# Optimization experiments

Hardware: AMD Instinct MI355X
Metric: run time of the kernel (lower is better)

## Reference

```python
import jax, jax.numpy as jnp
import numpy as np
from jax import lax

DIM = 64        # Branch(dim)
OUT = 2048      # TimesBlock out_channels == TTT model_dim
NH = 8          # num_heads
HD = OUT // NH  # 256 head dim
INNER = 4 * HD  # ttt_mlp hidden
MB = 10         # mini_batch_size
BASE_LR = 0.1   # ttt_base_lr
NK = 6          # TimesBlock num_kernels (k = 1,3,5,7,9,11)
LN_EPS = 1e-6


def _gelu(x):
    return jax.nn.gelu(x, approximate=False)


def _gelu_bwd(x):
    return 0.5 * (1.0 + lax.erf(x / jnp.sqrt(2.0))) + x * jnp.exp(-0.5 * x * x) / jnp.sqrt(2.0 * jnp.pi)


def _ttt_head(qs, ks, vs, W1h, b1h, W2h, b2h, gw, gb):
    # qs/ks/vs: [NC, MB, HD]; sequential scan over mini-batch chunks (TTT inner GD)
    eta = BASE_LR / MB

    def step(carry, chunk):
        W1c, b1c, W2c, b2c = carry
        xq, xk, xv = chunk
        Z1 = xk @ W1c + b1c              # [MB, INNER]
        A1 = _gelu(Z1)
        Z2 = A1 @ W2c + b2c              # [MB, HD]
        # grad of 0.5*||LN(Z2) - (xv - xk)||^2 wrt Z2 (fused LN l2 backward)
        tgt = xv - xk
        mu = Z2.mean(-1, keepdims=True)
        std = jnp.sqrt(Z2.var(-1, keepdims=True) + LN_EPS)
        xhat = (2 * 0 + Z2 - mu) / std
        gout = (gw * xhat + gb) - tgt
        gxh = gout * gw
        gZ2 = (gxh - gxh.mean(-1, keepdims=True) - xhat * (gxh * xhat).mean(-1, keepdims=True)) / std
        gZ1 = (gZ2 @ W2c.T) * _gelu_bwd(Z1)
        # inner-model SGD step
        W1n = W1c - eta * (xk.T @ gZ1)
        b1n = b1c - eta * gZ1.sum(0)
        W2n = W2c - eta * (A1.T @ gZ2)
        b2n = b2c - eta * gZ2.sum(0)
        # apply updated inner model to queries, post-LN + residual
        Z1q = xq @ W1n + b1n
        Z2q = _gelu(Z1q) @ W2n + b2n
        muq = Z2q.mean(-1, keepdims=True)
        stdq = jnp.sqrt(Z2q.var(-1, keepdims=True) + LN_EPS)
        out = xq + gw * ((Z2q - muq) / stdq) + gb
        return (W1n, b1n, W2n, b2n), out

    _, outs = lax.scan(step, (W1h, b1h, W2h, b2h), (qs, ks, vs))
    return outs.reshape(-1, HD)  # [T, HD]


def _forward(x, seg, conv_ws, conv_bs, wq, wk, wv, wo, W1, b1, W2, b2, ln_w, ln_b):
    B, T, C = x.shape
    xg = jnp.transpose(x, (0, 2, 1)).reshape(B, C, T // seg, seg)
    dn = ('NCHW', 'OIHW', 'NCHW')
    acc = 0.0
    for w, bc in zip(conv_ws, conv_bs):
        acc = acc + lax.conv_general_dilated(xg, w, (1, 1), 'SAME', dimension_numbers=dn) + bc[None, :, None, None]
    xb = acc / float(len(conv_ws))            # TimesBlock: mean over kernel ensemble
    xb = jax.nn.silu(xb)
    xb = jnp.transpose(xb.reshape(B, OUT, T), (0, 2, 1))  # [B, T, OUT]

    def heads(h):  # [B,T,OUT] -> [B,NH,NC,MB,HD]
        return jnp.transpose(h.reshape(B, T, NH, HD), (0, 2, 1, 3)).reshape(B, NH, T // MB, MB, HD)

    q = heads(xb @ wq.T)
    k = heads(xb @ wk.T)
    v = heads(xb @ wv.T)
    f = jax.vmap(jax.vmap(_ttt_head, in_axes=(0, 0, 0, 0, 0, 0, 0, 0, 0)),
                 in_axes=(0, 0, 0, None, None, None, None, None, None))
    o = f(q, k, v, W1, b1, W2, b2, ln_w, ln_b)  # [B, NH, T, HD]
    o = jnp.transpose(o, (0, 2, 1, 3)).reshape(B, T, OUT)
    return o @ wo.T


def setup_inputs() -> dict:
    key = jax.random.key(0)
    ks = jax.random.split(key, 24)
    B, T = 2, 400
    inp = {"x": jax.random.normal(ks[0], (B, T, DIM), jnp.float32), "seg": 20}
    for i in range(NK):
        kk = 2 * i + 1
        fan_out = OUT * kk * kk
        inp[f"conv_w{i}"] = jax.random.normal(ks[1 + i], (OUT, DIM, kk, kk), jnp.float32) * np.sqrt(2.0 / fan_out)
        inp[f"conv_b{i}"] = jnp.zeros((OUT,), jnp.float32)
    for j, nm in enumerate(["wq", "wk", "wv", "wo"]):
        inp[nm] = jax.random.normal(ks[8 + j], (OUT, OUT), jnp.float32) * 0.02
    inp["W1"] = jax.random.normal(ks[12], (NH, HD, INNER), jnp.float32) * 0.02
    inp["b1"] = jnp.zeros((NH, INNER), jnp.float32)
    inp["W2"] = jax.random.normal(ks[13], (NH, INNER, HD), jnp.float32) * 0.02
    inp["b2"] = jnp.zeros((NH, HD), jnp.float32)
    inp["ln_w"] = jnp.ones((NH, HD), jnp.float32)
    inp["ln_b"] = jnp.zeros((NH, HD), jnp.float32)
    return inp


def reference(x, seg, conv_w0, conv_b0, conv_w1, conv_b1, conv_w2, conv_b2,
              conv_w3, conv_b3, conv_w4, conv_b4, conv_w5, conv_b5,
              wq, wk, wv, wo, W1, b1, W2, b2, ln_w, ln_b):
    conv_ws = [conv_w0, conv_w1, conv_w2, conv_w3, conv_w4, conv_w5]
    conv_bs = [conv_b0, conv_b1, conv_b2, conv_b3, conv_b4, conv_b5]
    return _forward(x, seg, conv_ws, conv_bs, wq, wk, wv, wo, W1, b1, W2, b2, ln_w, ln_b)
```

## Files before the change

### kernel.cpp

```cpp
#include <hip/hip_runtime.h>


typedef __bf16 bf16x8 __attribute__((ext_vector_type(8)));
typedef float  f32x4  __attribute__((ext_vector_type(4)));

__device__ __forceinline__ unsigned short f2bf(float f){
  unsigned int u = __builtin_bit_cast(unsigned int, f);
  u += 0x7fffu + ((u >> 16) & 1u);
  return (unsigned short)(u >> 16);
}
__device__ __forceinline__ float bf2f(unsigned short b){
  unsigned int u = ((unsigned int)b) << 16;
  return __builtin_bit_cast(float, u);
}
__device__ __forceinline__ float gelu_f(float x){
  return 0.5f * x * (1.0f + erff(x * 0.70710678118654752f));
}
__device__ __forceinline__ float gelu_bwd_f(float x){
  return 0.5f * (1.0f + erff(x * 0.70710678118654752f))
       + x * __expf(-0.5f * x * x) * 0.3989422804014327f;
}

__device__ __forceinline__ float2 aload2(const float* p){
  unsigned long long v = __hip_atomic_load((const unsigned long long*)p,
                                           __ATOMIC_RELAXED, __HIP_MEMORY_SCOPE_AGENT);
  union { unsigned long long u; float2 f; } cv; cv.u = v; return cv.f;
}
__device__ __forceinline__ void aadd(float* p, float v){
  __hip_atomic_fetch_add(p, v, __ATOMIC_RELAXED, __HIP_MEMORY_SCOPE_AGENT);
}


__global__ __launch_bounds__(256) void k_weff(
    const float* __restrict__ w0, const float* __restrict__ w1,
    const float* __restrict__ w2, const float* __restrict__ w3,
    const float* __restrict__ w4, const float* __restrict__ w5,
    unsigned short* __restrict__ weff)
{
  extern __shared__ float sw[];
  const int off[6] = {0, 64, 640, 2240, 5376, 10560};
  const float* ws6[6] = {w0, w1, w2, w3, w4, w5};
  int o = blockIdx.x, tid = threadIdx.x;
#pragma unroll
  for (int i = 0; i < 6; i++){
    int kk = 2 * i + 1, sz = 64 * kk * kk;
    const float* src = ws6[i] + (size_t)o * sz;
    for (int idx = tid; idx < sz; idx += 256) sw[off[i] + idx] = src[idx];
  }
  __syncthreads();
  for (int t = tid; t < 7744; t += 256){
    int c = t / 121, dd = t % 121, di = dd / 11, dj = dd % 11;
    float s = 0.f;
#pragma unroll
    for (int i = 0; i < 6; i++){
      int kk = 2 * i + 1;
      int a = di - 5 + i, b = dj - 5 + i;
      if (a >= 0 && a < kk && b >= 0 && b < kk)
        s += sw[off[i] + (c * kk + a) * kk + b];
    }
    weff[(size_t)o * 7744 + t] = f2bf(s);
  }
}

__global__ __launch_bounds__(256) void k_im2col(
    const float* __restrict__ x, unsigned short* __restrict__ P)
{
  int idx = blockIdx.x * 256 + threadIdx.x;
  if (idx >= 800 * 7744) return;
  int n = idx / 7744, k = idx % 7744;
  int c = k / 121, dd = k % 121, di = dd / 11, dj = dd % 11;
  int b = n / 400, pos = n % 400, i = pos / 20, j = pos % 20;
  int ii = i + di - 5, jj = j + dj - 5;
  float v = 0.f;
  if (ii >= 0 && ii < 20 && jj >= 0 && jj < 20)
    v = x[((size_t)b * 400 + ii * 20 + jj) * 64 + c];
  P[idx] = f2bf(v);
}

__global__ __launch_bounds__(256) void k_wqkv(
    const float* __restrict__ wq, const float* __restrict__ wk,
    const float* __restrict__ wv, unsigned short* __restrict__ dst)
{
  int idx = blockIdx.x * 256 + threadIdx.x;
  if (idx >= 6144 * 2048) return;
  int m = idx >> 11, kk = idx & 2047;
  const float* src = (m < 2048) ? wq : ((m < 4096) ? wk : wv);
  dst[idx] = f2bf(src[(size_t)(m & 2047) * 2048 + kk]);
}

__global__ __launch_bounds__(256) void k_f2bf_copy(
    const float* __restrict__ src, unsigned short* __restrict__ dst, int n)
{
  int idx = blockIdx.x * 256 + threadIdx.x;
  if (idx < n) dst[idx] = f2bf(src[idx]);
}

__global__ __launch_bounds__(256) void k_bsum(
    const float* __restrict__ b0, const float* __restrict__ b1,
    const float* __restrict__ b2, const float* __restrict__ b3,
    const float* __restrict__ b4, const float* __restrict__ b5,
    float* __restrict__ bsum)
{
  int idx = blockIdx.x * 256 + threadIdx.x;
  if (idx < 2048)
    bsum[idx] = b0[idx] + b1[idx] + b2[idx] + b3[idx] + b4[idx] + b5[idx];
}

__global__ __launch_bounds__(256) void k_comb_silu(
    const float* __restrict__ p0, const float* __restrict__ p1,
    const float* __restrict__ bsum, unsigned short* __restrict__ xb)
{
  int i4 = (blockIdx.x * 256 + threadIdx.x) * 4;
  float4 a = *(const float4*)&p0[i4];
  float4 b = *(const float4*)&p1[i4];
  int mm = i4 & 2047;
  float4 bs = *(const float4*)&bsum[mm];
  float v[4] = {a.x + b.x + bs.x, a.y + b.y + bs.y, a.z + b.z + bs.z, a.w + b.w + bs.w};
  ushort4 o;
#pragma unroll
  for (int i = 0; i < 4; i++){
    float t = v[i] * (1.0f / 6.0f);
    float sv = t / (1.0f + __expf(-t));
    ((unsigned short*)&o)[i] = f2bf(sv);
  }
  *(ushort4*)&xb[i4] = o;
}

__global__ __launch_bounds__(256) void k_comb_add4(
    const float* __restrict__ p, float* __restrict__ out)
{
  int i4 = (blockIdx.x * 256 + threadIdx.x) * 4;
  float4 a = *(const float4*)&p[i4];
  float4 b = *(const float4*)&p[1638400 + i4];
  float4 c = *(const float4*)&p[3276800 + i4];
  float4 d = *(const float4*)&p[4915200 + i4];
  float4 o = {a.x + b.x + c.x + d.x, a.y + b.y + c.y + d.y,
              a.z + b.z + c.z + d.z, a.w + b.w + c.w + d.w};
  *(float4*)&out[i4] = o;
}

template<int MODE>
__global__ __launch_bounds__(256, 1) void k_gemm(
    const unsigned short* __restrict__ A, const unsigned short* __restrict__ B,
    int M, int N, int lda, int ldb, int kLen,
    unsigned short* __restrict__ qb, unsigned short* __restrict__ kb,
    unsigned short* __restrict__ vb, float* __restrict__ outf)
{
  __shared__ unsigned short As[128 * 32];
  __shared__ unsigned short Bs[128 * 32];
  int tid = threadIdx.x, w = tid >> 6, l = tid & 63, qd = l >> 4, lm = l & 15;
  int m0 = blockIdx.x * 128, n0 = blockIdx.y * 128;
  int kBase = blockIdx.z * kLen;

  f32x4 acc[4][4];
#pragma unroll
  for (int i = 0; i < 4; i++)
#pragma unroll
    for (int j = 0; j < 4; j++){ acc[i][j][0]=0.f; acc[i][j][1]=0.f; acc[i][j][2]=0.f; acc[i][j][3]=0.f; }

  int nk = kLen >> 5;
  for (int kt = 0; kt < nk; kt++){
    int k0 = kBase + (kt << 5);
#pragma unroll
    for (int i = 0; i < 2; i++){
      int cidx = tid + i * 256;
      int row = cidx >> 2, kc = (cidx & 3) << 3;
      *(uint4*)&As[row * 32 + kc] = *(const uint4*)&A[(size_t)(m0 + row) * lda + k0 + kc];
      int br = n0 + row; if (br >= N) br = N - 1;
      *(uint4*)&Bs[row * 32 + kc] = *(const uint4*)&B[(size_t)br * ldb + k0 + kc];
    }
    __syncthreads();
    bf16x8 af[4], bfv[4];
#pragma unroll
    for (int i = 0; i < 4; i++)
      af[i] = *(const bf16x8*)&As[((w >> 1) * 64 + i * 16 + lm) * 32 + qd * 8];
#pragma unroll
    for (int j = 0; j < 4; j++)
      bfv[j] = *(const bf16x8*)&Bs[((w & 1) * 64 + j * 16 + lm) * 32 + qd * 8];
#pragma unroll
    for (int i = 0; i < 4; i++)
#pragma unroll
      for (int j = 0; j < 4; j++)
        acc[i][j] = __builtin_amdgcn_mfma_f32_16x16x32_bf16(af[i], bfv[j], acc[i][j], 0, 0, 0);
    __syncthreads();
  }

#pragma unroll
  for (int i = 0; i < 4; i++){
    int mBase = m0 + (w >> 1) * 64 + i * 16 + qd * 4;
#pragma unroll
    for (int j = 0; j < 4; j++){
      int n = n0 + (w & 1) * 64 + j * 16 + lm;
      if (n < N){
#pragma unroll
        for (int rr = 0; rr < 4; rr++){
          float val = acc[i][j][rr];
          int mm = mBase + rr;
          if (MODE == 1){
            int proj = mm >> 11, o = mm & 2047, hh = o >> 8, d = o & 255;
            int bh = (n / 400) * 8 + hh, tt = n % 400;
            unsigned short* dst = (proj == 0) ? qb : ((proj == 1) ? kb : vb);
            dst[((size_t)bh * 400 + tt) * 256 + d] = f2bf(val);
          } else {
            outf[(size_t)blockIdx.z * M * N + (size_t)n * M + mm] = val;
          }
        }
      }
    }
  }
}

#define O_W1BT 0
#define O_W2K  16896
#define O_W2N  33792
#define O_XKQ  52224
#define O_TGT  54864
#define O_A1   57424
#define O_A1T  58144
#define O_GZ2  60192
#define O_GZ1  62832
#define O_XQ2  64880
#define O_GZ2T 67520
#define O_XKT  73664
#define O_A1Q  79808
#define O_F32  80528
#define O_GW   81168
#define O_GB   81424
#define US_TOTAL 81680
#define TTT_LDS_BYTES (81680 * 2)

#define ETA 0.01f
#define BAR_STRIDE 32

__global__ __launch_bounds__(256, 1) void k_ttt(
    const unsigned short* __restrict__ qg, const unsigned short* __restrict__ kg,
    const unsigned short* __restrict__ vg,
    const float* __restrict__ W1g, const float* __restrict__ b1g,
    const float* __restrict__ W2g, const float* __restrict__ b2g,
    const float* __restrict__ gwg, const float* __restrict__ gbg,
    float* __restrict__ z2acc, unsigned short* __restrict__ zqp,
    unsigned int* __restrict__ bar)
{
  extern __shared__ unsigned short lds[];
  float* ldsf = (float*)&lds[O_F32];

  int tid = threadIdx.x, w = tid >> 6, l = tid & 63, qd = l >> 4, lm = l & 15;
  int bid = blockIdx.x;
  int jj = bid >> 3, xx = bid & 7;
  int h  = xx + 8 * (jj >> 4);
  int sl = jj & 15;
  int hh = h & 7;

  for (int i = tid; i < US_TOTAL; i += 256) lds[i] = 0;
  __syncthreads();

  float w1r[4][4][4];
#pragma unroll
  for (int a = 0; a < 4; a++)
#pragma unroll
    for (int nt = 0; nt < 4; nt++)
#pragma unroll
      for (int rr = 0; rr < 4; rr++)
        w1r[a][nt][rr] = W1g[((size_t)hh * 256 + (4 * w + a) * 16 + qd * 4 + rr) * 1024
                             + sl * 64 + nt * 16 + lm];
  float w2r[16][4];
#pragma unroll
  for (int nt = 0; nt < 16; nt++)
#pragma unroll
    for (int rr = 0; rr < 4; rr++)
      w2r[nt][rr] = W2g[((size_t)hh * 1024 + sl * 64 + w * 16 + qd * 4 + rr) * 256
                        + nt * 16 + lm];
  if (tid < 64)  ldsf[tid] = b1g[hh * 1024 + sl * 64 + tid];
  if (tid < 256){
    ldsf[64 + tid] = b2g[hh * 256 + tid];
    lds[O_GW + tid] = f2bf(gwg[hh * 256 + tid]);
    lds[O_GB + tid] = f2bf(gbg[hh * 256 + tid]);
  }

#define WRITE_W1BF() do { \
  _Pragma("unroll") for (int a = 0; a < 4; a++){ \
    int m0i = (4 * w + a) * 16 + qd * 4; \
    _Pragma("unroll") for (int nt = 0; nt < 4; nt++){ \
      int n = nt * 16 + lm; \
      unsigned int p0 = f2bf(w1r[a][nt][0]) | ((unsigned int)f2bf(w1r[a][nt][1]) << 16); \
      unsigned int p1 = f2bf(w1r[a][nt][2]) | ((unsigned int)f2bf(w1r[a][nt][3]) << 16); \
      *(unsigned int*)&lds[O_W1BT + n * 264 + m0i]     = p0; \
      *(unsigned int*)&lds[O_W1BT + n * 264 + m0i + 2] = p1; \
    } } } while(0)

#define WRITE_W2BF() do { \
  int mB = w * 16 + qd * 4; \
  _Pragma("unroll") for (int nt = 0; nt < 16; nt++){ \
    int n = nt * 16 + lm; \
    _Pragma("unroll") for (int rr = 0; rr < 4; rr++) \
      lds[O_W2K + (mB + rr) * 264 + n] = f2bf(w2r[nt][rr]); \
    unsigned int p0 = f2bf(w2r[nt][0]) | ((unsigned int)f2bf(w2r[nt][1]) << 16); \
    unsigned int p1 = f2bf(w2r[nt][2]) | ((unsigned int)f2bf(w2r[nt][3]) << 16); \
    *(unsigned int*)&lds[O_W2N + n * 72 + mB]     = p0; \
    *(unsigned int*)&lds[O_W2N + n * 72 + mB + 2] = p1; \
  } } while(0)

  const size_t hb2 = (size_t)h * 400 * 256;

#define LOAD_XK_TGT(NCH) do { \
  const unsigned int* kp = (const unsigned int*)(kg + hb2 + (size_t)(NCH) * 2560); \
  const unsigned int* vp = (const unsigned int*)(vg + hb2 + (size_t)(NCH) * 2560); \
  _Pragma("unroll") for (int i5 = 0; i5 < 5; i5++){ \
    int f2i = i5 * 256 + tid; \
    unsigned int ku = kp[f2i], vu = vp[f2i]; \
    int row = f2i >> 7, col = (f2i & 127) * 2; \
    *(unsigned int*)&lds[O_XKQ + row * 264 + col] = ku; \
    lds[O_XKT + col * 24 + row]       = (unsigned short)(ku & 0xffffu); \
    lds[O_XKT + (col + 1) * 24 + row] = (unsigned short)(ku >> 16); \
    float kv0 = bf2f((unsigned short)(ku & 0xffffu)), kv1 = bf2f((unsigned short)(ku >> 16)); \
    float vv0 = bf2f((unsigned short)(vu & 0xffffu)), vv1 = bf2f((unsigned short)(vu >> 16)); \
    unsigned int tu = (unsigned int)f2bf(vv0 - kv0) | ((unsigned int)f2bf(vv1 - kv1) << 16); \
    *(unsigned int*)&lds[O_TGT + row * 256 + col] = tu; \
  } } while(0)

#define LOAD_XQ(NCH) do { \
  const unsigned int* qp = (const unsigned int*)(qg + hb2 + (size_t)(NCH) * 2560); \
  _Pragma("unroll") for (int i5 = 0; i5 < 5; i5++){ \
    int f2i = i5 * 256 + tid; \
    unsigned int qu = qp[f2i]; \
    int row = f2i >> 7, col = (f2i & 127) * 2; \
    *(unsigned int*)&lds[O_XQ2 + row * 264 + col] = qu; \
  } } while(0)

  WRITE_W1BF();
  WRITE_W2BF();
  LOAD_XK_TGT(0);
  LOAD_XQ(0);
  __syncthreads();

  for (int nch = 0; nch < 40; nch++){
    const size_t chunkBase = (size_t)(h * 40 + nch) * 10 * 256;

    f32x4 z1a; z1a[0]=0.f; z1a[1]=0.f; z1a[2]=0.f; z1a[3]=0.f;
#pragma unroll
    for (int ks = 0; ks < 8; ks++){
      bf16x8 av = *(const bf16x8*)&lds[O_XKQ + lm * 264 + ks * 32 + qd * 8];
      bf16x8 bv = *(const bf16x8*)&lds[O_W1BT + (w * 16 + lm) * 264 + ks * 32 + qd * 8];
      z1a = __builtin_amdgcn_mfma_f32_16x16x32_bf16(av, bv, z1a, 0, 0, 0);
    }
    float z1v[4];
    {
      float b1n = ldsf[w * 16 + lm];
#pragma unroll
      for (int rr = 0; rr < 4; rr++){
        z1v[rr] = z1a[rr] + b1n;
        int mr = qd * 4 + rr;
        if (mr < 10){
          float a1 = gelu_f(z1v[rr]);
          unsigned short ab = f2bf(a1);
          lds[O_A1 + mr * 72 + w * 16 + lm] = ab;
          lds[O_A1T + (w * 16 + lm) * 32 + mr] = ab;
        }
      }
    }
    __syncthreads();

#pragma unroll
    for (int nt4 = 0; nt4 < 4; nt4++){
      int nt = 4 * w + nt4;
      f32x4 p; p[0]=0.f; p[1]=0.f; p[2]=0.f; p[3]=0.f;
#pragma unroll
      for (int ks = 0; ks < 2; ks++){
        bf16x8 av = *(const bf16x8*)&lds[O_A1 + lm * 72 + ks * 32 + qd * 8];
        bf16x8 bv = *(const bf16x8*)&lds[O_W2N + (nt * 16 + lm) * 72 + ks * 32 + qd * 8];
        p = __builtin_amdgcn_mfma_f32_16x16x32_bf16(av, bv, p, 0, 0, 0);
      }
#pragma unroll
      for (int rr = 0; rr < 4; rr++){
        int mr = qd * 4 + rr;
        if (mr < 10)
          aadd(&z2acc[chunkBase + (size_t)mr * 256 + nt * 16 + lm], p[rr]);
      }
    }
    __syncthreads();

    if (tid == 0)
      __hip_atomic_fetch_add(bar + h * BAR_STRIDE, 1u, __ATOMIC_RELAXED, __HIP_MEMORY_SCOPE_AGENT);

    if (nch > 0){
      f32x4 zq; zq[0]=0.f; zq[1]=0.f; zq[2]=0.f; zq[3]=0.f;
#pragma unroll
      for (int ks = 0; ks < 8; ks++){
        bf16x8 av = *(const bf16x8*)&lds[O_XQ2 + lm * 264 + ks * 32 + qd * 8];
        bf16x8 bv = *(const bf16x8*)&lds[O_W1BT + (w * 16 + lm) * 264 + ks * 32 + qd * 8];
        zq = __builtin_amdgcn_mfma_f32_16x16x32_bf16(av, bv, zq, 0, 0, 0);
      }
      float b1n = ldsf[w * 16 + lm];
#pragma unroll
      for (int rr = 0; rr < 4; rr++){
        int mr = qd * 4 + rr;
        if (mr < 10)
          lds[O_A1Q + mr * 72 + w * 16 + lm] = f2bf(gelu_f(zq[rr] + b1n));
      }
    }
    __syncthreads();

    if (nch > 0){
      LOAD_XQ(nch);
      unsigned short* zq_out = zqp + ((size_t)(h * 16 + sl) * 40 + (nch - 1)) * 2560;
#pragma unroll
      for (int nt4 = 0; nt4 < 4; nt4++){
        int nt = 4 * w + nt4;
        f32x4 p; p[0]=0.f; p[1]=0.f; p[2]=0.f; p[3]=0.f;
#pragma unroll
        for (int ks = 0; ks < 2; ks++){
          bf16x8 av = *(const bf16x8*)&lds[O_A1Q + lm * 72 + ks * 32 + qd * 8];
          bf16x8 bv = *(const bf16x8*)&lds[O_W2N + (nt * 16 + lm) * 72 + ks * 32 + qd * 8];
          p = __builtin_amdgcn_mfma_f32_16x16x32_bf16(av, bv, p, 0, 0, 0);
        }
        float bb = (sl == 0) ? ldsf[64 + nt * 16 + lm] : 0.f;
#pragma unroll
        for (int rr = 0; rr < 4; rr++){
          int mr = qd * 4 + rr;
          if (mr < 10)
            zq_out[mr * 256 + nt * 16 + lm] = f2bf(p[rr] + bb);
        }
      }
    }

    if (tid == 0){
      unsigned int target = 16u * (unsigned int)(nch + 1);
      unsigned int spins = 0;
      while (__hip_atomic_load(bar + h * BAR_STRIDE, __ATOMIC_RELAXED, __HIP_MEMORY_SCOPE_AGENT) < target
             && spins < 8000000u){ spins++; __builtin_amdgcn_s_sleep(1); }
    }
    __syncthreads();

    for (int r2 = w; r2 < 10; r2 += 4){
      int c0 = l * 4;
      const float* bp = &z2acc[chunkBase + (size_t)r2 * 256 + c0];
      float2 u01 = aload2(bp);
      float2 u23 = aload2(bp + 2);
      float zz[4] = {u01.x, u01.y, u23.x, u23.y};
      float s1 = 0.f, s2 = 0.f;
#pragma unroll
      for (int i = 0; i < 4; i++){ zz[i] += ldsf[64 + c0 + i]; s1 += zz[i]; s2 += zz[i] * zz[i]; }
#pragma unroll
      for (int off = 32; off >= 1; off >>= 1){ s1 += __shfl_xor(s1, off, 64); s2 += __shfl_xor(s2, off, 64); }
      float mu = s1 * (1.f / 256.f);
      float var = s2 * (1.f / 256.f) - mu * mu;
      float rstd = rsqrtf(var + 1e-6f);
      float xh[4], gx[4];
      float t1 = 0.f, t2 = 0.f;
#pragma unroll
      for (int i = 0; i < 4; i++){
        xh[i] = (zz[i] - mu) * rstd;
        float gwv = bf2f(lds[O_GW + c0 + i]), gbv = bf2f(lds[O_GB + c0 + i]);
        float tg = bf2f(lds[O_TGT + r2 * 256 + c0 + i]);
        float go = gwv * xh[i] + gbv - tg;
        gx[i] = go * gwv;
        t1 += gx[i]; t2 += gx[i] * xh[i];
      }
#pragma unroll
      for (int off = 32; off >= 1; off >>= 1){ t1 += __shfl_xor(t1, off, 64); t2 += __shfl_xor(t2, off, 64); }
      float m1 = t1 * (1.f / 256.f), m2 = t2 * (1.f / 256.f);
      float g0 = (gx[0] - m1 - xh[0] * m2) * rstd;
      float g1 = (gx[1] - m1 - xh[1] * m2) * rstd;
      float g2 = (gx[2] - m1 - xh[2] * m2) * rstd;
      float g3 = (gx[3] - m1 - xh[3] * m2) * rstd;
      unsigned int p0 = f2bf(g0) | ((unsigned int)f2bf(g1) << 16);
      unsigned int p1 = f2bf(g2) | ((unsigned int)f2bf(g3) << 16);
      *(unsigned int*)&lds[O_GZ2 + r2 * 264 + c0]     = p0;
      *(unsigned int*)&lds[O_GZ2 + r2 * 264 + c0 + 2] = p1;
    }
    __syncthreads();

    {
      float sum = 0.f;
#pragma unroll
      for (int r2 = 0; r2 < 10; r2++){
        unsigned short g = lds[O_GZ2 + r2 * 264 + tid];
        lds[O_GZ2T + tid * 24 + r2] = g;
        sum += bf2f(g);
      }
      ldsf[64 + tid] -= ETA * sum;
    }
    {
      f32x4 g1a; g1a[0]=0.f; g1a[1]=0.f; g1a[2]=0.f; g1a[3]=0.f;
#pragma unroll
      for (int ks = 0; ks < 8; ks++){
        bf16x8 av = *(const bf16x8*)&lds[O_GZ2 + lm * 264 + ks * 32 + qd * 8];
        bf16x8 bv = *(const bf16x8*)&lds[O_W2K + (w * 16 + lm) * 264 + ks * 32 + qd * 8];
        g1a = __builtin_amdgcn_mfma_f32_16x16x32_bf16(av, bv, g1a, 0, 0, 0);
      }
#pragma unroll
      for (int rr = 0; rr < 4; rr++){
        int mr = qd * 4 + rr;
        if (mr < 10){
          float gz1 = g1a[rr] * gelu_bwd_f(z1v[rr]);
          lds[O_GZ1 + (w * 16 + lm) * 32 + mr] = f2bf(gz1);
        }
      }
    }
    __syncthreads();

    if (tid < 64){
      float sum = 0.f;
#pragma unroll
      for (int kx = 0; kx < 10; kx++) sum += bf2f(lds[O_GZ1 + tid * 32 + kx]);
      ldsf[tid] -= ETA * sum;
    }
#pragma unroll
    for (int a = 0; a < 4; a++){
      int mt = 4 * w + a;
      bf16x8 av = *(const bf16x8*)&lds[O_XKT + (mt * 16 + lm) * 24 + (qd & 1) * 8];
#pragma unroll
      for (int nt = 0; nt < 4; nt++){
        bf16x8 bv = *(const bf16x8*)&lds[O_GZ1 + (nt * 16 + lm) * 32 + qd * 8];
        f32x4 d; d[0]=0.f; d[1]=0.f; d[2]=0.f; d[3]=0.f;
        d = __builtin_amdgcn_mfma_f32_16x16x32_bf16(av, bv, d, 0, 0, 0);
#pragma unroll
        for (int rr = 0; rr < 4; rr++) w1r[a][nt][rr] -= ETA * d[rr];
      }
    }
    {
      bf16x8 av2 = *(const bf16x8*)&lds[O_A1T + (w * 16 + lm) * 32 + qd * 8];
#pragma unroll
      for (int nt = 0; nt < 16; nt++){
        bf16x8 bv = *(const bf16x8*)&lds[O_GZ2T + (nt * 16 + lm) * 24 + (qd & 1) * 8];
        f32x4 d; d[0]=0.f; d[1]=0.f; d[2]=0.f; d[3]=0.f;
        d = __builtin_amdgcn_mfma_f32_16x16x32_bf16(av2, bv, d, 0, 0, 0);
#pragma unroll
        for (int rr = 0; rr < 4; rr++) w2r[nt][rr] -= ETA * d[rr];
      }
    }
    WRITE_W1BF();
    WRITE_W2BF();
    __syncthreads();

    if (nch + 1 < 40){
      LOAD_XK_TGT(nch + 1);
    }
    __syncthreads();
  }

  {
    f32x4 zq; zq[0]=0.f; zq[1]=0.f; zq[2]=0.f; zq[3]=0.f;
#pragma unroll
    for (int ks = 0; ks < 8; ks++){
      bf16x8 av = *(const bf16x8*)&lds[O_XQ2 + lm * 264 + ks * 32 + qd * 8];
      bf16x8 bv = *(const bf16x8*)&lds[O_W1BT + (w * 16 + lm) * 264 + ks * 32 + qd * 8];
      zq = __builtin_amdgcn_mfma_f32_16x16x32_bf16(av, bv, zq, 0, 0, 0);
    }
    float b1n = ldsf[w * 16 + lm];
#pragma unroll
    for (int rr = 0; rr < 4; rr++){
      int mr = qd * 4 + rr;
      if (mr < 10)
        lds[O_A1Q + mr * 72 + w * 16 + lm] = f2bf(gelu_f(zq[rr] + b1n));
    }
  }
  __syncthreads();
  {
    unsigned short* zq_out = zqp + ((size_t)(h * 16 + sl) * 40 + 39) * 2560;
#pragma unroll
    for (int nt4 = 0; nt4 < 4; nt4++){
      int nt = 4 * w + nt4;
      f32x4 p; p[0]=0.f; p[1]=0.f; p[2]=0.f; p[3]=0.f;
#pragma unroll
      for (int ks = 0; ks < 2; ks++){
        bf16x8 av = *(const bf16x8*)&lds[O_A1Q + lm * 72 + ks * 32 + qd * 8];
        bf16x8 bv = *(const bf16x8*)&lds[O_W2N + (nt * 16 + lm) * 72 + ks * 32 + qd * 8];
        p = __builtin_amdgcn_mfma_f32_16x16x32_bf16(av, bv, p, 0, 0, 0);
      }
      float bb = (sl == 0) ? ldsf[64 + nt * 16 + lm] : 0.f;
#pragma unroll
      for (int rr = 0; rr < 4; rr++){
        int mr = qd * 4 + rr;
        if (mr < 10)
          zq_out[mr * 256 + nt * 16 + lm] = f2bf(p[rr] + bb);
      }
    }
  }
}

__global__ __launch_bounds__(256) void k_lnout(
    const unsigned short* __restrict__ zqp, const unsigned short* __restrict__ qg,
    const float* __restrict__ gwg, const float* __restrict__ gbg,
    unsigned short* __restrict__ obf)
{
  int w = threadIdx.x >> 6, l = threadIdx.x & 63;
  int gr = blockIdx.x * 4 + w;
  int h = gr / 400, t = gr % 400, hh = h & 7, b = h >> 3;
  int nch = t / 10, mr = t % 10;
  int c0 = l * 4;
  float z[4] = {0.f, 0.f, 0.f, 0.f};
#pragma unroll
  for (int sl = 0; sl < 16; sl++){
    const unsigned short* zp = zqp + (((size_t)(h * 16 + sl) * 40 + nch) * 10 + mr) * 256 + c0;
    ushort4 u = *(const ushort4*)zp;
    z[0] += bf2f(u.x); z[1] += bf2f(u.y); z[2] += bf2f(u.z); z[3] += bf2f(u.w);
  }
  float s1 = 0.f, s2 = 0.f;
#pragma unroll
  for (int i = 0; i < 4; i++){ s1 += z[i]; s2 += z[i] * z[i]; }
#pragma unroll
  for (int off = 32; off >= 1; off >>= 1){ s1 += __shfl_xor(s1, off, 64); s2 += __shfl_xor(s2, off, 64); }
  float mu = s1 * (1.f / 256.f);
  float var = s2 * (1.f / 256.f) - mu * mu;
  float rstd = rsqrtf(var + 1e-6f);
  const unsigned short* qp = &qg[((size_t)h * 400 + t) * 256];
  ushort4 qu = *(const ushort4*)&qp[c0];
  float qv[4] = {bf2f(qu.x), bf2f(qu.y), bf2f(qu.z), bf2f(qu.w)};
  unsigned short* op = &obf[((size_t)(b * 400 + t)) * 2048 + hh * 256];
#pragma unroll
  for (int i = 0; i < 4; i++){
    float xh = (z[i] - mu) * rstd;
    float o = qv[i] + gwg[hh * 256 + c0 + i] * xh + gbg[hh * 256 + c0 + i];
    op[c0 + i] = f2bf(o);
  }
}

#define WS_WEFF   0u
#define WS_P      31719424u
#define WS_WQKV   44109824u
#define WS_WOB    52428800u
#define WS_Z2ACC  62722048u
#define WS_XB     69275648u
#define WS_Q      72552448u
#define WS_K      75829248u
#define WS_V      79106048u
#define WS_OBF    82382848u
#define WS_BSUM   85659648u
#define WS_BAR    85667840u

extern "C" void kernel_launch(void* const* d_in, const int* in_sizes, int n_in,
                              void* d_out, int out_size, void* d_ws, size_t ws_size,
                              hipStream_t stream)
{
  (void)in_sizes; (void)n_in; (void)out_size; (void)ws_size;
  const float* x  = (const float*)d_in[0];
  const float* cw[6]; const float* cb[6];
  for (int i = 0; i < 6; i++){ cw[i] = (const float*)d_in[2 + 2 * i]; cb[i] = (const float*)d_in[3 + 2 * i]; }
  const float* wq  = (const float*)d_in[14];
  const float* wk  = (const float*)d_in[15];
  const float* wv  = (const float*)d_in[16];
  const float* wo  = (const float*)d_in[17];
  const float* W1  = (const float*)d_in[18];
  const float* b1  = (const float*)d_in[19];
  const float* W2  = (const float*)d_in[20];
  const float* b2  = (const float*)d_in[21];
  const float* lnw = (const float*)d_in[22];
  const float* lnb = (const float*)d_in[23];
  float* outf = (float*)d_out;

  char* wsb = (char*)d_ws;
  unsigned short* weff = (unsigned short*)(wsb + WS_WEFF);
  unsigned short* P    = (unsigned short*)(wsb + WS_P);
  unsigned short* wqkv = (unsigned short*)(wsb + WS_WQKV);
  unsigned short* wob  = (unsigned short*)(wsb + WS_WOB);
  unsigned short* xb   = (unsigned short*)(wsb + WS_XB);
  unsigned short* qb   = (unsigned short*)(wsb + WS_Q);
  unsigned short* kb   = (unsigned short*)(wsb + WS_K);
  unsigned short* vb   = (unsigned short*)(wsb + WS_V);
  float* z2acc = (float*)(wsb + WS_Z2ACC);
  unsigned short* zqp = (unsigned short*)(wsb + WS_WEFF);
  unsigned short* obf = (unsigned short*)(wsb + WS_OBF);
  float* bsum = (float*)(wsb + WS_BSUM);
  unsigned int* bar = (unsigned int*)(wsb + WS_BAR);
  float* g0part = (float*)(wsb + WS_Q);
  float* g2part = (float*)(wsb + WS_WEFF);

  hipMemsetAsync(bar, 0, 16 * BAR_STRIDE * 4, stream);
  hipFuncSetAttribute(reinterpret_cast<const void*>(k_ttt),
                      hipFuncAttributeMaxDynamicSharedMemorySize, TTT_LDS_BYTES);
  hipFuncSetAttribute(reinterpret_cast<const void*>(k_weff),
                      hipFuncAttributeMaxDynamicSharedMemorySize, 18304 * 4);

  k_weff<<<2048, 256, 18304 * 4, stream>>>(cw[0], cw[1], cw[2], cw[3], cw[4], cw[5], weff);
  k_im2col<<<(800 * 7744 + 255) / 256, 256, 0, stream>>>(x, P);
  k_wqkv<<<(6144 * 2048 + 255) / 256, 256, 0, stream>>>(wq, wk, wv, wqkv);
  k_bsum<<<8, 256, 0, stream>>>(cb[0], cb[1], cb[2], cb[3], cb[4], cb[5], bsum);

  k_gemm<2><<<dim3(16, 7, 2), 256, 0, stream>>>(weff, P, 2048, 800, 7744, 7744, 3872,
                                                nullptr, nullptr, nullptr, g0part);
  k_comb_silu<<<1600, 256, 0, stream>>>(g0part, g0part + 1638400, bsum, xb);

  k_gemm<1><<<dim3(48, 7, 1), 256, 0, stream>>>(wqkv, xb, 6144, 800, 2048, 2048, 2048,
                                                qb, kb, vb, nullptr);

  k_f2bf_copy<<<(2048 * 2048 + 255) / 256, 256, 0, stream>>>(wo, wob, 2048 * 2048);
  hipMemsetAsync(z2acc, 0, 16 * 40 * 10 * 256 * 4, stream);

  k_ttt<<<256, 256, TTT_LDS_BYTES, stream>>>(qb, kb, vb, W1, b1, W2, b2, lnw, lnb,
                                             z2acc, zqp, bar);
  k_lnout<<<1600, 256, 0, stream>>>(zqp, qb, lnw, lnb, obf);

  k_gemm<2><<<dim3(16, 7, 4), 256, 0, stream>>>(wob, obf, 2048, 800, 2048, 2048, 512,
                                                nullptr, nullptr, nullptr, g2part);
  k_comb_add4<<<1600, 256, 0, stream>>>(g2part, outf);
}
```

Before: 1.101 ms.

## Replace Z2 atomic accumulation with double-buffered bf16 partials and prefetch next chunk

Each of the 16 slice blocks per head now writes its partial Z2 tile as bf16 into a double-buffered per-slice slot. The reducing block sums the 16 partials itself, replacing the fp32 atomic adds into a global accumulator and dropping the memset of that buffer. Next-chunk K/V loads are issued into registers early so they overlap the compute, and W1/W2 MFMA fragments are hoisted into registers and reused across the key and query GEMMs. A1T and GZ1 LDS indices are XOR-swizzled to cut bank conflicts. The trade-offs are lower precision from bf16 partial sums, more global reads in the reduction, and higher register pressure.

```diff
diff --git a/kernel.cpp b/kernel.cpp
--- a/kernel.cpp
+++ b/kernel.cpp
@@ -19,15 +19,6 @@
 __device__ __forceinline__ float gelu_bwd_f(float x){
   return 0.5f * (1.0f + erff(x * 0.70710678118654752f))
        + x * __expf(-0.5f * x * x) * 0.3989422804014327f;
-}
-
-__device__ __forceinline__ float2 aload2(const float* p){
-  unsigned long long v = __hip_atomic_load((const unsigned long long*)p,
-                                           __ATOMIC_RELAXED, __HIP_MEMORY_SCOPE_AGENT);
-  union { unsigned long long u; float2 f; } cv; cv.u = v; return cv.f;
-}
-__device__ __forceinline__ void aadd(float* p, float v){
-  __hip_atomic_fetch_add(p, v, __ATOMIC_RELAXED, __HIP_MEMORY_SCOPE_AGENT);
 }
 
 
@@ -229,8 +220,12 @@
 #define US_TOTAL 81680
 #define TTT_LDS_BYTES (81680 * 2)
 
+#define A1T_IDX(r, c) (O_A1T + ((((r) * 32) + (c)) ^ (((r) & 3) << 3)))
+#define GZ1_IDX(r, c) (O_GZ1 + ((((r) * 32) + (c)) ^ (((r) & 3) << 3)))
+
 #define ETA 0.01f
 #define BAR_STRIDE 32
+#define PPAR 655360
 
 __global__ __launch_bounds__(256, 1) void k_ttt(
     const unsigned short* __restrict__ qg, const unsigned short* __restrict__ kg,
@@ -238,7 +233,7 @@
     const float* __restrict__ W1g, const float* __restrict__ b1g,
     const float* __restrict__ W2g, const float* __restrict__ b2g,
     const float* __restrict__ gwg, const float* __restrict__ gbg,
-    float* __restrict__ z2acc, unsigned short* __restrict__ zqp,
+    unsigned short* __restrict__ part, unsigned short* __restrict__ zqp,
     unsigned int* __restrict__ bar)
 {
   extern __shared__ unsigned short lds[];
@@ -302,12 +297,20 @@
 
   const size_t hb2 = (size_t)h * 400 * 256;
 
-#define LOAD_XK_TGT(NCH) do { \
+  unsigned int kreg[5], vreg[5];
+
+#define LOAD_XK_REGS(NCH) do { \
   const unsigned int* kp = (const unsigned int*)(kg + hb2 + (size_t)(NCH) * 2560); \
   const unsigned int* vp = (const unsigned int*)(vg + hb2 + (size_t)(NCH) * 2560); \
   _Pragma("unroll") for (int i5 = 0; i5 < 5; i5++){ \
+    kreg[i5] = kp[i5 * 256 + tid]; \
+    vreg[i5] = vp[i5 * 256 + tid]; \
+  } } while(0)
+
+#define COMMIT_XK_TGT() do { \
+  _Pragma("unroll") for (int i5 = 0; i5 < 5; i5++){ \
     int f2i = i5 * 256 + tid; \
-    unsigned int ku = kp[f2i], vu = vp[f2i]; \
+    unsigned int ku = kreg[i5], vu = vreg[i5]; \
     int row = f2i >> 7, col = (f2i & 127) * 2; \
     *(unsigned int*)&lds[O_XKQ + row * 264 + col] = ku; \
     lds[O_XKT + col * 24 + row]       = (unsigned short)(ku & 0xffffu); \
@@ -329,52 +332,64 @@
 
   WRITE_W1BF();
   WRITE_W2BF();
-  LOAD_XK_TGT(0);
+  LOAD_XK_REGS(0);
+  COMMIT_XK_TGT();
   LOAD_XQ(0);
   __syncthreads();
 
   for (int nch = 0; nch < 40; nch++){
-    const size_t chunkBase = (size_t)(h * 40 + nch) * 10 * 256;
+    bf16x8 w1f[8];
+#pragma unroll
+    for (int ks = 0; ks < 8; ks++)
+      w1f[ks] = *(const bf16x8*)&lds[O_W1BT + (w * 16 + lm) * 264 + ks * 32 + qd * 8];
+    float b1n = ldsf[w * 16 + lm];
 
     f32x4 z1a; z1a[0]=0.f; z1a[1]=0.f; z1a[2]=0.f; z1a[3]=0.f;
 #pragma unroll
     for (int ks = 0; ks < 8; ks++){
       bf16x8 av = *(const bf16x8*)&lds[O_XKQ + lm * 264 + ks * 32 + qd * 8];
-      bf16x8 bv = *(const bf16x8*)&lds[O_W1BT + (w * 16 + lm) * 264 + ks * 32 + qd * 8];
-      z1a = __builtin_amdgcn_mfma_f32_16x16x32_bf16(av, bv, z1a, 0, 0, 0);
+      z1a = __builtin_amdgcn_mfma_f32_16x16x32_bf16(av, w1f[ks], z1a, 0, 0, 0);
     }
     float z1v[4];
+#pragma unroll
+    for (int rr = 0; rr < 4; rr++){
+      z1v[rr] = z1a[rr] + b1n;
+      int mr = qd * 4 + rr;
+      if (mr < 10){
+        float a1 = gelu_f(z1v[rr]);
+        unsigned short ab = f2bf(a1);
+        lds[O_A1 + mr * 72 + w * 16 + lm] = ab;
+        lds[A1T_IDX(w * 16 + lm, mr)] = ab;
+      }
+    }
+    __syncthreads();
+
+    bf16x8 a1f[2], w2f[4][2];
+#pragma unroll
+    for (int ks = 0; ks < 2; ks++)
+      a1f[ks] = *(const bf16x8*)&lds[O_A1 + lm * 72 + ks * 32 + qd * 8];
+#pragma unroll
+    for (int nt4 = 0; nt4 < 4; nt4++)
+#pragma unroll
+      for (int ks = 0; ks < 2; ks++)
+        w2f[nt4][ks] = *(const bf16x8*)&lds[O_W2N + ((4 * w + nt4) * 16 + lm) * 72 + ks * 32 + qd * 8];
+
     {
-      float b1n = ldsf[w * 16 + lm];
-#pragma unroll
-      for (int rr = 0; rr < 4; rr++){
-        z1v[rr] = z1a[rr] + b1n;
-        int mr = qd * 4 + rr;
-        if (mr < 10){
-          float a1 = gelu_f(z1v[rr]);
-          unsigned short ab = f2bf(a1);
-          lds[O_A1 + mr * 72 + w * 16 + lm] = ab;
-          lds[O_A1T + (w * 16 + lm) * 32 + mr] = ab;
+      unsigned short* pslot = part + ((nch & 1) ? PPAR : 0) + (size_t)(h * 16 + sl) * 2560;
+#pragma unroll
+      for (int nt4 = 0; nt4 < 4; nt4++){
+        int nt = 4 * w + nt4;
+        f32x4 p; p[0]=0.f; p[1]=0.f; p[2]=0.f; p[3]=0.f;
+#pragma unroll
+        for (int ks = 0; ks < 2; ks++)
+          p = __builtin_amdgcn_mfma_f32_16x16x32_bf16(a1f[ks], w2f[nt4][ks], p, 0, 0, 0);
+#pragma unroll
+        for (int rr = 0; rr < 4; rr++){
+          int mr = qd * 4 + rr;
+          if (mr < 10)
+            __hip_atomic_store(&pslot[mr * 256 + nt * 16 + lm], f2bf(p[rr]),
+                               __ATOMIC_RELAXED, __HIP_MEMORY_SCOPE_AGENT);
         }
-      }
-    }
-    __syncthreads();
-
-#pragma unroll
-    for (int nt4 = 0; nt4 < 4; nt4++){
-      int nt = 4 * w + nt4;
-      f32x4 p; p[0]=0.f; p[1]=0.f; p[2]=0.f; p[3]=0.f;
-#pragma unroll
-      for (int ks = 0; ks < 2; ks++){
-        bf16x8 av = *(const bf16x8*)&lds[O_A1 + lm * 72 + ks * 32 + qd * 8];
-        bf16x8 bv = *(const bf16x8*)&lds[O_W2N + (nt * 16 + lm) * 72 + ks * 32 + qd * 8];
-        p = __builtin_amdgcn_mfma_f32_16x16x32_bf16(av, bv, p, 0, 0, 0);
-      }
-#pragma unroll
-      for (int rr = 0; rr < 4; rr++){
-        int mr = qd * 4 + rr;
-        if (mr < 10)
-          aadd(&z2acc[chunkBase + (size_t)mr * 256 + nt * 16 + lm], p[rr]);
       }
     }
     __syncthreads();
@@ -382,15 +397,16 @@
     if (tid == 0)
       __hip_atomic_fetch_add(bar + h * BAR_STRIDE, 1u, __ATOMIC_RELAXED, __HIP_MEMORY_SCOPE_AGENT);
 
+    if (nch + 1 < 40)
+      LOAD_XK_REGS(nch + 1);
+
     if (nch > 0){
       f32x4 zq; zq[0]=0.f; zq[1]=0.f; zq[2]=0.f; zq[3]=0.f;
 #pragma unroll
       for (int ks = 0; ks < 8; ks++){
         bf16x8 av = *(const bf16x8*)&lds[O_XQ2 + lm * 264 + ks * 32 + qd * 8];
-        bf16x8 bv = *(const bf16x8*)&lds[O_W1BT + (w * 16 + lm) * 264 + ks * 32 + qd * 8];
-        zq = __builtin_amdgcn_mfma_f32_16x16x32_bf16(av, bv, zq, 0, 0, 0);
-      }
-      float b1n = ldsf[w * 16 + lm];
+        zq = __builtin_amdgcn_mfma_f32_16x16x32_bf16(av, w1f[ks], zq, 0, 0, 0);
+      }
 #pragma unroll
       for (int rr = 0; rr < 4; rr++){
         int mr = qd * 4 + rr;
@@ -403,16 +419,17 @@
     if (nch > 0){
       LOAD_XQ(nch);
       unsigned short* zq_out = zqp + ((size_t)(h * 16 + sl) * 40 + (nch - 1)) * 2560;
+      bf16x8 a1qf[2];
+#pragma unroll
+      for (int ks = 0; ks < 2; ks++)
+        a1qf[ks] = *(const bf16x8*)&lds[O_A1Q + lm * 72 + ks * 32 + qd * 8];
 #pragma unroll
       for (int nt4 = 0; nt4 < 4; nt4++){
         int nt = 4 * w + nt4;
         f32x4 p; p[0]=0.f; p[1]=0.f; p[2]=0.f; p[3]=0.f;
 #pragma unroll
-        for (int ks = 0; ks < 2; ks++){
-          bf16x8 av = *(const bf16x8*)&lds[O_A1Q + lm * 72 + ks * 32 + qd * 8];
-          bf16x8 bv = *(const bf16x8*)&lds[O_W2N + (nt * 16 + lm) * 72 + ks * 32 + qd * 8];
-          p = __builtin_amdgcn_mfma_f32_16x16x32_bf16(av, bv, p, 0, 0, 0);
-        }
+        for (int ks = 0; ks < 2; ks++)
+          p = __builtin_amdgcn_mfma_f32_16x16x32_bf16(a1qf[ks], w2f[nt4][ks], p, 0, 0, 0);
         float bb = (sl == 0) ? ldsf[64 + nt * 16 + lm] : 0.f;
 #pragma unroll
         for (int rr = 0; rr < 4; rr++){
@@ -431,42 +448,54 @@
     }
     __syncthreads();
 
-    for (int r2 = w; r2 < 10; r2 += 4){
-      int c0 = l * 4;
-      const float* bp = &z2acc[chunkBase + (size_t)r2 * 256 + c0];
-      float2 u01 = aload2(bp);
-      float2 u23 = aload2(bp + 2);
-      float zz[4] = {u01.x, u01.y, u23.x, u23.y};
-      float s1 = 0.f, s2 = 0.f;
-#pragma unroll
-      for (int i = 0; i < 4; i++){ zz[i] += ldsf[64 + c0 + i]; s1 += zz[i]; s2 += zz[i] * zz[i]; }
-#pragma unroll
-      for (int off = 32; off >= 1; off >>= 1){ s1 += __shfl_xor(s1, off, 64); s2 += __shfl_xor(s2, off, 64); }
-      float mu = s1 * (1.f / 256.f);
-      float var = s2 * (1.f / 256.f) - mu * mu;
-      float rstd = rsqrtf(var + 1e-6f);
-      float xh[4], gx[4];
-      float t1 = 0.f, t2 = 0.f;
-#pragma unroll
-      for (int i = 0; i < 4; i++){
-        xh[i] = (zz[i] - mu) * rstd;
-        float gwv = bf2f(lds[O_GW + c0 + i]), gbv = bf2f(lds[O_GB + c0 + i]);
-        float tg = bf2f(lds[O_TGT + r2 * 256 + c0 + i]);
-        float go = gwv * xh[i] + gbv - tg;
-        gx[i] = go * gwv;
-        t1 += gx[i]; t2 += gx[i] * xh[i];
-      }
-#pragma unroll
-      for (int off = 32; off >= 1; off >>= 1){ t1 += __shfl_xor(t1, off, 64); t2 += __shfl_xor(t2, off, 64); }
-      float m1 = t1 * (1.f / 256.f), m2 = t2 * (1.f / 256.f);
-      float g0 = (gx[0] - m1 - xh[0] * m2) * rstd;
-      float g1 = (gx[1] - m1 - xh[1] * m2) * rstd;
-      float g2 = (gx[2] - m1 - xh[2] * m2) * rstd;
-      float g3 = (gx[3] - m1 - xh[3] * m2) * rstd;
-      unsigned int p0 = f2bf(g0) | ((unsigned int)f2bf(g1) << 16);
-      unsigned int p1 = f2bf(g2) | ((unsigned int)f2bf(g3) << 16);
-      *(unsigned int*)&lds[O_GZ2 + r2 * 264 + c0]     = p0;
-      *(unsigned int*)&lds[O_GZ2 + r2 * 264 + c0 + 2] = p1;
+    {
+      const unsigned long long* pb = (const unsigned long long*)
+          (part + ((nch & 1) ? PPAR : 0) + (size_t)h * 16 * 2560);
+      for (int r2 = w; r2 < 10; r2 += 4){
+        int c0 = l * 4;
+        float zz[4];
+#pragma unroll
+        for (int i = 0; i < 4; i++) zz[i] = ldsf[64 + c0 + i];
+#pragma unroll
+        for (int s16 = 0; s16 < 16; s16++){
+          unsigned long long u = __hip_atomic_load(&pb[(size_t)s16 * 640 + r2 * 64 + l],
+                                                   __ATOMIC_RELAXED, __HIP_MEMORY_SCOPE_AGENT);
+          zz[0] += bf2f((unsigned short)(u & 0xffffu));
+          zz[1] += bf2f((unsigned short)((u >> 16) & 0xffffu));
+          zz[2] += bf2f((unsigned short)((u >> 32) & 0xffffu));
+          zz[3] += bf2f((unsigned short)(u >> 48));
+        }
+        float s1 = 0.f, s2 = 0.f;
+#pragma unroll
+        for (int i = 0; i < 4; i++){ s1 += zz[i]; s2 += zz[i] * zz[i]; }
+#pragma unroll
+        for (int off = 32; off >= 1; off >>= 1){ s1 += __shfl_xor(s1, off, 64); s2 += __shfl_xor(s2, off, 64); }
+        float mu = s1 * (1.f / 256.f);
+        float var = s2 * (1.f / 256.f) - mu * mu;
+        float rstd = rsqrtf(var + 1e-6f);
+        float xh[4], gx[4];
+        float t1 = 0.f, t2 = 0.f;
+#pragma unroll
+        for (int i = 0; i < 4; i++){
+          xh[i] = (zz[i] - mu) * rstd;
+          float gwv = bf2f(lds[O_GW + c0 + i]), gbv = bf2f(lds[O_GB + c0 + i]);
+          float tg = bf2f(lds[O_TGT + r2 * 256 + c0 + i]);
+          float go = gwv * xh[i] + gbv - tg;
+          gx[i] = go * gwv;
+          t1 += gx[i]; t2 += gx[i] * xh[i];
+        }
+#pragma unroll
+        for (int off = 32; off >= 1; off >>= 1){ t1 += __shfl_xor(t1, off, 64); t2 += __shfl_xor(t2, off, 64); }
+        float m1 = t1 * (1.f / 256.f), m2 = t2 * (1.f / 256.f);
+        float g0 = (gx[0] - m1 - xh[0] * m2) * rstd;
+        float g1 = (gx[1] - m1 - xh[1] * m2) * rstd;
+        float g2 = (gx[2] - m1 - xh[2] * m2) * rstd;
+        float g3 = (gx[3] - m1 - xh[3] * m2) * rstd;
+        unsigned int p0 = f2bf(g0) | ((unsigned int)f2bf(g1) << 16);
+        unsigned int p1 = f2bf(g2) | ((unsigned int)f2bf(g3) << 16);
+        *(unsigned int*)&lds[O_GZ2 + r2 * 264 + c0]     = p0;
+        *(unsigned int*)&lds[O_GZ2 + r2 * 264 + c0 + 2] = p1;
+      }
     }
     __syncthreads();
 
@@ -493,7 +522,7 @@
         int mr = qd * 4 + rr;
         if (mr < 10){
           float gz1 = g1a[rr] * gelu_bwd_f(z1v[rr]);
-          lds[O_GZ1 + (w * 16 + lm) * 32 + mr] = f2bf(gz1);
+          lds[GZ1_IDX(w * 16 + lm, mr)] = f2bf(gz1);
         }
       }
     }
@@ -502,7 +531,7 @@
     if (tid < 64){
       float sum = 0.f;
 #pragma unroll
-      for (int kx = 0; kx < 10; kx++) sum += bf2f(lds[O_GZ1 + tid * 32 + kx]);
+      for (int kx = 0; kx < 10; kx++) sum += bf2f(lds[GZ1_IDX(tid, kx)]);
       ldsf[tid] -= ETA * sum;
     }
 #pragma unroll
@@ -511,7 +540,7 @@
       bf16x8 av = *(const bf16x8*)&lds[O_XKT + (mt * 16 + lm) * 24 + (qd & 1) * 8];
 #pragma unroll
       for (int nt = 0; nt < 4; nt++){
-        bf16x8 bv = *(const bf16x8*)&lds[O_GZ1 + (nt * 16 + lm) * 32 + qd * 8];
+        bf16x8 bv = *(const bf16x8*)&lds[GZ1_IDX(nt * 16 + lm, qd * 8)];
         f32x4 d; d[0]=0.f; d[1]=0.f; d[2]=0.f; d[3]=0.f;
         d = __builtin_amdgcn_mfma_f32_16x16x32_bf16(av, bv, d, 0, 0, 0);
 #pragma unroll
@@ -519,7 +548,7 @@
       }
     }
     {
-      bf16x8 av2 = *(const bf16x8*)&lds[O_A1T + (w * 16 + lm) * 32 + qd * 8];
+      bf16x8 av2 = *(const bf16x8*)&lds[A1T_IDX(w * 16 + lm, qd * 8)];
 #pragma unroll
       for (int nt = 0; nt < 16; nt++){
         bf16x8 bv = *(const bf16x8*)&lds[O_GZ2T + (nt * 16 + lm) * 24 + (qd & 1) * 8];
@@ -534,7 +563,7 @@
     __syncthreads();
 
     if (nch + 1 < 40){
-      LOAD_XK_TGT(nch + 1);
+      COMMIT_XK_TGT();
     }
     __syncthreads();
   }
@@ -658,7 +687,7 @@
   unsigned short* qb   = (unsigned short*)(wsb + WS_Q);
   unsigned short* kb   = (unsigned short*)(wsb + WS_K);
   unsigned short* vb   = (unsigned short*)(wsb + WS_V);
-  float* z2acc = (float*)(wsb + WS_Z2ACC);
+  unsigned short* part = (unsigned short*)(wsb + WS_Z2ACC);
   unsigned short* zqp = (unsigned short*)(wsb + WS_WEFF);
   unsigned short* obf = (unsigned short*)(wsb + WS_OBF);
   float* bsum = (float*)(wsb + WS_BSUM);
@@ -685,10 +714,9 @@
                                                 qb, kb, vb, nullptr);
 
   k_f2bf_copy<<<(2048 * 2048 + 255) / 256, 256, 0, stream>>>(wo, wob, 2048 * 2048);
-  hipMemsetAsync(z2acc, 0, 16 * 40 * 10 * 256 * 4, stream);
 
   k_ttt<<<256, 256, TTT_LDS_BYTES, stream>>>(qb, kb, vb, W1, b1, W2, b2, lnw, lnb,
-                                             z2acc, zqp, bar);
+                                             part, zqp, bar);
   k_lnout<<<1600, 256, 0, stream>>>(zqp, qb, lnw, lnb, obf);
 
   k_gemm<2><<<dim3(16, 7, 4), 256, 0, stream>>>(wob, obf, 2048, 800, 2048, 2048, 512,
```

After: 1.154 ms. 1.05x slower.
